# Optimization experiments

Hardware: AMD Instinct MI355X
Metric: run time of the kernel (lower is better)

## Reference

```python
import jax, jax.numpy as jnp
import numpy as np

N = 250_000
E = 8_000_000
EPS = 1e-5


def _bn(x, gamma, beta):
    # BatchNorm1d in training mode: batch stats over dim 0, biased variance
    mu = x.mean(axis=0)
    var = x.var(axis=0)
    return (x - mu) * jax.lax.rsqrt(var + EPS) * gamma + beta


def setup_inputs() -> dict:
    key = jax.random.key(0)
    ks = jax.random.split(key, 24)
    f32 = jnp.float32
    inp = {
        'pos': jax.random.normal(ks[0], (N, 2), f32),
        'vel': jax.random.normal(ks[1], (N, 2), f32),
        'edge_index': jax.random.randint(ks[2], (2, E), 0, N, jnp.int32),
        'lin_in_w': jax.random.normal(ks[3], (4, 4), f32) * 0.5,
        'lin_in_b': jax.random.normal(ks[4], (4,), f32) * 0.1,
        'msg_w1': jax.random.normal(ks[5], (8, 8), f32) * 0.35,
        'msg_b1': jax.random.normal(ks[6], (8,), f32) * 0.1,
        'msg_g1': jax.random.uniform(ks[7], (8,), f32, 0.5, 1.5),
        'msg_be1': jax.random.normal(ks[8], (8,), f32) * 0.1,
        'msg_w2': jax.random.normal(ks[9], (8, 4), f32) * 0.35,
        'msg_b2': jax.random.normal(ks[10], (4,), f32) * 0.1,
        'msg_g2': jax.random.uniform(ks[11], (4,), f32, 0.5, 1.5),
        'msg_be2': jax.random.normal(ks[12], (4,), f32) * 0.1,
        'upd_w1': jax.random.normal(ks[13], (8, 8), f32) * 0.35,
        'upd_b1': jax.random.normal(ks[14], (8,), f32) * 0.1,
        'upd_g1': jax.random.uniform(ks[15], (8,), f32, 0.5, 1.5),
        'upd_be1': jax.random.normal(ks[16], (8,), f32) * 0.1,
        'upd_w2': jax.random.normal(ks[17], (8, 4), f32) * 0.35,
        'upd_b2': jax.random.normal(ks[18], (4,), f32) * 0.1,
        'upd_g2': jax.random.uniform(ks[19], (4,), f32, 0.5, 1.5),
        'upd_be2': jax.random.normal(ks[20], (4,), f32) * 0.1,
        'pred_w': jax.random.normal(ks[21], (4, 2), f32) * 0.5,
        'pred_b': jax.random.normal(ks[22], (2,), f32) * 0.1,
    }
    return inp


def reference(pos, vel, edge_index,
              lin_in_w, lin_in_b,
              msg_w1, msg_b1, msg_g1, msg_be1,
              msg_w2, msg_b2, msg_g2, msg_be2,
              upd_w1, upd_b1, upd_g1, upd_be1,
              upd_w2, upd_b2, upd_g2, upd_be2,
              pred_w, pred_b):
    n = pos.shape[0]
    # input projection: h = lin_in(cat(pos, vel))  -> [N, 4]
    h = jnp.concatenate([pos, vel], axis=-1) @ lin_in_w + lin_in_b

    # PyG source_to_target: j = source = edge_index[0], i = target = edge_index[1]
    src, dst = edge_index[0], edge_index[1]
    h_i = h[dst]  # [E, 4]
    h_j = h[src]  # [E, 4]

    # message MLP on cat(h_i, h_j): Linear->BN->Tanh->Linear->BN->Tanh
    m = jnp.concatenate([h_i, h_j], axis=-1)            # [E, 8]
    m = jnp.tanh(_bn(m @ msg_w1 + msg_b1, msg_g1, msg_be1))
    m = jnp.tanh(_bn(m @ msg_w2 + msg_b2, msg_g2, msg_be2))  # [E, 4]

    # zero out messages where h_i == h_j exactly (self-like edges)
    zero_diff = jnp.all(h_i == h_j, axis=1)             # [E]
    m = jnp.where(zero_diff[:, None], 0.0, m)

    # aggregate: scatter-add on first half, scatter-mean on second half
    add_out = jax.ops.segment_sum(m[:, :2], dst, num_segments=n)   # [N, 2]
    sum_out = jax.ops.segment_sum(m[:, 2:], dst, num_segments=n)   # [N, 2]
    cnt = jax.ops.segment_sum(jnp.ones((m.shape[0],), m.dtype), dst, num_segments=n)
    mean_out = sum_out / jnp.maximum(cnt, 1.0)[:, None]
    aggr = jnp.concatenate([add_out, mean_out], axis=1)  # [N, 4]

    # update MLP on cat(h, aggr)
    u = jnp.concatenate([h, aggr], axis=-1)              # [N, 8]
    u = jnp.tanh(_bn(u @ upd_w1 + upd_b1, upd_g1, upd_be1))
    u = jnp.tanh(_bn(u @ upd_w2 + upd_b2, upd_g2, upd_be2))  # [N, 4]

    return u @ pred_w + pred_b                           # [N, 2]
```

## Files before the change

kernel.cpp:

```cpp
#include <hip/hip_runtime.h>

#define EPSBN 1e-5f
#define NB 512
#define GB 256
#define CAP 18000

typedef float vf4 __attribute__((ext_vector_type(4)));
typedef _Float16 vh8 __attribute__((ext_vector_type(8)));
typedef unsigned int uint32;

__device__ __forceinline__ float ftanh(float x) {
    return 1.0f - 2.0f / (__expf(2.0f * x) + 1.0f);
}

__device__ __forceinline__ float wave_sum(float v) {
#pragma unroll
    for (int off = 32; off > 0; off >>= 1) v += __shfl_down(v, off);
    return v;
}

__device__ __forceinline__ void z1_of(const float4 hi, const float4 hj,
                                      const float* __restrict__ w, const float* __restrict__ b,
                                      float* z) {
#pragma unroll
    for (int j = 0; j < 8; ++j) {
        z[j] = b[j]
             + hi.x * w[0 * 8 + j] + hi.y * w[1 * 8 + j] + hi.z * w[2 * 8 + j] + hi.w * w[3 * 8 + j]
             + hj.x * w[4 * 8 + j] + hj.y * w[5 * 8 + j] + hj.z * w[6 * 8 + j] + hj.w * w[7 * 8 + j];
    }
}

__device__ __forceinline__ void mat8x4(const float* u, const float* w,
                                       const float* b, float* z) {
#pragma unroll
    for (int c = 0; c < 4; ++c) {
        float t = b[c];
#pragma unroll
        for (int k = 0; k < 8; ++k) t += u[k] * w[k * 4 + c];
        z[c] = t;
    }
}

__device__ __forceinline__ void mat8x8(const float* u, const float* __restrict__ w,
                                       const float* __restrict__ b, float* z) {
#pragma unroll
    for (int j = 0; j < 8; ++j) {
        float t = b[j];
#pragma unroll
        for (int k = 0; k < 8; ++k) t += u[k] * w[k * 8 + j];
        z[j] = t;
    }
}

template <int NV>
__device__ __forceinline__ void block_reduce_atomics(float* a, float* __restrict__ sums) {
    __shared__ float red[NV * 4];
    int wid = threadIdx.x >> 6, lane = threadIdx.x & 63;
#pragma unroll
    for (int i = 0; i < NV; ++i) {
        float v = wave_sum(a[i]);
        if (lane == 0) red[i * 4 + wid] = v;
    }
    __syncthreads();
    if (threadIdx.x < NV) {
        float v = red[threadIdx.x * 4 + 0] + red[threadIdx.x * 4 + 1]
                + red[threadIdx.x * 4 + 2] + red[threadIdx.x * 4 + 3];
        atomicAdd(&sums[threadIdx.x], v);
    }
}

__device__ __forceinline__ void fin_lds(const float* __restrict__ sums,
                                        const float* __restrict__ g, const float* __restrict__ be,
                                        int d, float inv, float* out) {
    int j = threadIdx.x;
    if (j < d) {
        float mu = sums[j] * inv;
        float var = sums[d + j] * inv - mu * mu;
        float s = g[j] * rsqrtf(var + EPSBN);
        out[j] = s;
        out[d + j] = be[j] - mu * s;
    }
    __syncthreads();
}

__device__ __forceinline__ void stats1_edge(float4 hi, float4 hj,
                                            const float* __restrict__ w1, const float* __restrict__ b1,
                                            float* a) {
    float z[8];
    z1_of(hi, hj, w1, b1, z);
#pragma unroll
    for (int j = 0; j < 8; ++j) { a[j] += z[j]; a[8 + j] += z[j] * z[j]; }
}

__device__ __forceinline__ vf4 z2_edge(float4 hi, float4 hj,
                                       const float* __restrict__ w1, const float* __restrict__ b1,
                                       const float* ss1,
                                       const float* __restrict__ w2, const float* __restrict__ b2) {
    float z[8], m1[8], z2[4];
    z1_of(hi, hj, w1, b1, z);
#pragma unroll
    for (int j = 0; j < 8; ++j) m1[j] = ftanh(z[j] * ss1[j] + ss1[8 + j]);
    mat8x4(m1, w2, b2, z2);
    vf4 r = {z2[0], z2[1], z2[2], z2[3]};
    return r;
}

__device__ __forceinline__ void stats2_edge(float4 hi, float4 hj,
                                            const float* __restrict__ w1, const float* __restrict__ b1,
                                            const float* ss1,
                                            const float* __restrict__ w2, const float* __restrict__ b2,
                                            float* a) {
    vf4 q = z2_edge(hi, hj, w1, b1, ss1, w2, b2);
    a[0] += q.x; a[4] += q.x * q.x;
    a[1] += q.y; a[5] += q.y * q.y;
    a[2] += q.z; a[6] += q.z * q.z;
    a[3] += q.w; a[7] += q.w * q.w;
}

__device__ __forceinline__ void m1_ofh(vf4 ziA, vf4 ziB, vh8 zjh, float* m1) {
    m1[0] = ftanh(ziA.x + (float)zjh[0]); m1[1] = ftanh(ziA.y + (float)zjh[1]);
    m1[2] = ftanh(ziA.z + (float)zjh[2]); m1[3] = ftanh(ziA.w + (float)zjh[3]);
    m1[4] = ftanh(ziB.x + (float)zjh[4]); m1[5] = ftanh(ziB.y + (float)zjh[5]);
    m1[6] = ftanh(ziB.z + (float)zjh[6]); m1[7] = ftanh(ziB.w + (float)zjh[7]);
}

__global__ __launch_bounds__(256) void k_h(const float* __restrict__ pos, const float* __restrict__ vel,
                                           const float* __restrict__ w, const float* __restrict__ b,
                                           float4* __restrict__ h, int n) {
    int i = blockIdx.x * blockDim.x + threadIdx.x;
    if (i >= n) return;
    float2 p = ((const float2*)pos)[i];
    float2 v = ((const float2*)vel)[i];
    float o[4];
#pragma unroll
    for (int d = 0; d < 4; ++d)
        o[d] = b[d] + p.x * w[0 * 4 + d] + p.y * w[1 * 4 + d] + v.x * w[2 * 4 + d] + v.y * w[3 * 4 + d];
    h[i] = make_float4(o[0], o[1], o[2], o[3]);
}

__global__ __launch_bounds__(256) void k_zt(const float4* __restrict__ h,
                                            const float* __restrict__ w1, const float* __restrict__ b1,
                                            vf4* __restrict__ zi, vf4* __restrict__ zj, int n) {
    int i = blockIdx.x * blockDim.x + threadIdx.x;
    if (i >= n) return;
    float4 hv = h[i];
    float zi8[8], zj8[8];
#pragma unroll
    for (int j = 0; j < 8; ++j) {
        zi8[j] = hv.x * w1[0 * 8 + j] + hv.y * w1[1 * 8 + j] + hv.z * w1[2 * 8 + j] + hv.w * w1[3 * 8 + j];
        zj8[j] = b1[j]
               + hv.x * w1[4 * 8 + j] + hv.y * w1[5 * 8 + j] + hv.z * w1[6 * 8 + j] + hv.w * w1[7 * 8 + j];
    }
    vf4 a = {zi8[0], zi8[1], zi8[2], zi8[3]};
    vf4 b_ = {zi8[4], zi8[5], zi8[6], zi8[7]};
    vf4 c = {zj8[0], zj8[1], zj8[2], zj8[3]};
    vf4 d = {zj8[4], zj8[5], zj8[6], zj8[7]};
    zi[2 * (size_t)i] = a; zi[2 * (size_t)i + 1] = b_;
    zj[2 * (size_t)i] = c; zj[2 * (size_t)i + 1] = d;
}

__global__ __launch_bounds__(256) void k_fold(vf4* __restrict__ zi, const vf4* __restrict__ zj,
                                              vh8* __restrict__ zjH,
                                              const float* __restrict__ sums1,
                                              const float* __restrict__ g1, const float* __restrict__ be1,
                                              float invE, int n) {
    __shared__ float ss1[16];
    fin_lds(sums1, g1, be1, 8, invE, ss1);
    int i = blockIdx.x * blockDim.x + threadIdx.x;
    if (i >= n) return;
    vf4 a = zi[2 * (size_t)i], b = zi[2 * (size_t)i + 1];
    a.x *= ss1[0]; a.y *= ss1[1]; a.z *= ss1[2]; a.w *= ss1[3];
    b.x *= ss1[4]; b.y *= ss1[5]; b.z *= ss1[6]; b.w *= ss1[7];
    zi[2 * (size_t)i] = a; zi[2 * (size_t)i + 1] = b;
    vf4 c = zj[2 * (size_t)i], d = zj[2 * (size_t)i + 1];
    vh8 hpk;
    hpk[0] = (_Float16)(c.x * ss1[0] + ss1[8]);
    hpk[1] = (_Float16)(c.y * ss1[1] + ss1[9]);
    hpk[2] = (_Float16)(c.z * ss1[2] + ss1[10]);
    hpk[3] = (_Float16)(c.w * ss1[3] + ss1[11]);
    hpk[4] = (_Float16)(d.x * ss1[4] + ss1[12]);
    hpk[5] = (_Float16)(d.y * ss1[5] + ss1[13]);
    hpk[6] = (_Float16)(d.z * ss1[6] + ss1[14]);
    hpk[7] = (_Float16)(d.w * ss1[7] + ss1[15]);
    zjH[i] = hpk;
}

__global__ void k_foldw(const float* __restrict__ sums2,
                        const float* __restrict__ g2, const float* __restrict__ be2, float invE,
                        const float* __restrict__ w2, const float* __restrict__ b2,
                        float* __restrict__ w2f, float* __restrict__ b2f) {
    __shared__ float ss2[8];
    int j = threadIdx.x;
    if (j < 4) {
        float mu = sums2[j] * invE;
        float var = sums2[4 + j] * invE - mu * mu;
        float s = g2[j] * rsqrtf(var + EPSBN);
        ss2[j] = s;
        ss2[4 + j] = be2[j] - mu * s;
    }
    __syncthreads();
    if (j < 32) w2f[j] = w2[j] * ss2[j & 3];
    if (j < 4)  b2f[j] = b2[j] * ss2[j] + ss2[4 + j];
}

__global__ __launch_bounds__(256, 2) void k_cnt(const int* __restrict__ idx, const float4* __restrict__ h,
                                                const float* __restrict__ w1, const float* __restrict__ b1,
                                                uint32* __restrict__ cntmat, float* __restrict__ sums,
                                                int E_, int T) {
    __shared__ uint32 hist[NB];
    for (int b = threadIdx.x; b < NB; b += 256) hist[b] = 0;
    float a[16];
#pragma unroll
    for (int i = 0; i < 16; ++i) a[i] = 0.f;
    __syncthreads();
    int lo = blockIdx.x * T, hi2 = min(E_, lo + T);
    for (int e0 = lo + 4 * threadIdx.x; e0 < hi2; e0 += 1024) {
        int m = min(4, hi2 - e0);
        if (m == 4) {
            int s0 = __builtin_nontemporal_load(idx + e0);
            int s1 = __builtin_nontemporal_load(idx + e0 + 1);
            int s2 = __builtin_nontemporal_load(idx + e0 + 2);
            int s3 = __builtin_nontemporal_load(idx + e0 + 3);
            int d0 = __builtin_nontemporal_load(idx + E_ + e0);
            int d1 = __builtin_nontemporal_load(idx + E_ + e0 + 1);
            int d2 = __builtin_nontemporal_load(idx + E_ + e0 + 2);
            int d3 = __builtin_nontemporal_load(idx + E_ + e0 + 3);
            float4 hi0 = h[d0], hj0 = h[s0];
            float4 hi1 = h[d1], hj1 = h[s1];
            float4 hi2 = h[d2], hj2 = h[s2];
            float4 hi3 = h[d3], hj3 = h[s3];
            atomicAdd(&hist[d0 >> 9], 1u);
            atomicAdd(&hist[d1 >> 9], 1u);
            atomicAdd(&hist[d2 >> 9], 1u);
            atomicAdd(&hist[d3 >> 9], 1u);
            stats1_edge(hi0, hj0, w1, b1, a);
            stats1_edge(hi1, hj1, w1, b1, a);
            stats1_edge(hi2, hj2, w1, b1, a);
            stats1_edge(hi3, hj3, w1, b1, a);
        } else {
            for (int k = 0; k < m; ++k) {
                int s = __builtin_nontemporal_load(idx + e0 + k);
                int d = __builtin_nontemporal_load(idx + E_ + e0 + k);
                float4 hi = h[d], hj = h[s];
                atomicAdd(&hist[d >> 9], 1u);
                stats1_edge(hi, hj, w1, b1, a);
            }
        }
    }
    __syncthreads();
    for (int b = threadIdx.x; b < NB; b += 256)
        cntmat[(size_t)b * GB + blockIdx.x] = hist[b];
    block_reduce_atomics<16>(a, sums);
}

__device__ __forceinline__ void scan256(uint32 v, uint32* excl_out, uint32* total) {
    __shared__ uint32 ts[256];
    ts[threadIdx.x] = v;
    __syncthreads();
    for (int off = 1; off < 256; off <<= 1) {
        uint32 t = (threadIdx.x >= (uint32)off) ? ts[threadIdx.x - off] : 0u;
        __syncthreads();
        ts[threadIdx.x] += t;
        __syncthreads();
    }
    *excl_out = ts[threadIdx.x] - v;
    *total = ts[255];
}

__device__ __forceinline__ void scan512(uint32* v, uint32* excl_out, uint32* total) {
    __shared__ uint32 ts[256];
    uint32 local = v[0] + v[1];
    ts[threadIdx.x] = local;
    __syncthreads();
    for (int off = 1; off < 256; off <<= 1) {
        uint32 t = (threadIdx.x >= (uint32)off) ? ts[threadIdx.x - off] : 0u;
        __syncthreads();
        ts[threadIdx.x] += t;
        __syncthreads();
    }
    *excl_out = ts[threadIdx.x] - local;
    *total = ts[255];
}

__global__ __launch_bounds__(256) void k_scanA(uint32* __restrict__ cntmat, uint32* __restrict__ rowtot) {
    size_t base = (size_t)blockIdx.x * GB + threadIdx.x;
    uint32 v = cntmat[base];
    uint32 excl, tot;
    scan256(v, &excl, &tot);
    cntmat[base] = excl;
    if (threadIdx.x == 0) rowtot[blockIdx.x] = tot;
}

__global__ __launch_bounds__(256) void k_scanB(const uint32* __restrict__ rowtot, uint32* __restrict__ bbase) {
    uint32 v[2];
    v[0] = rowtot[threadIdx.x * 2]; v[1] = rowtot[threadIdx.x * 2 + 1];
    uint32 excl, tot;
    scan512(v, &excl, &tot);
    bbase[threadIdx.x * 2] = excl;
    bbase[threadIdx.x * 2 + 1] = excl + v[0];
    if (threadIdx.x == 0) bbase[NB] = tot;
}

__global__ __launch_bounds__(256) void k_reorder(const int* __restrict__ idx,
                                                 const uint32* __restrict__ cntmat, const uint32* __restrict__ bbase,
                                                 uint32* __restrict__ sp, int E_, int T) {
    __shared__ uint32 cur[NB];
    for (int b = threadIdx.x; b < NB; b += 256)
        cur[b] = bbase[b] + cntmat[(size_t)b * GB + blockIdx.x];
    __syncthreads();
    int lo = blockIdx.x * T, hi2 = min(E_, lo + T);
    for (int e0 = lo + 4 * threadIdx.x; e0 < hi2; e0 += 1024) {
        int m = min(4, hi2 - e0);
        if (m == 4) {
            int s0 = __builtin_nontemporal_load(idx + e0);
            int s1 = __builtin_nontemporal_load(idx + e0 + 1);
            int s2 = __builtin_nontemporal_load(idx + e0 + 2);
            int s3 = __builtin_nontemporal_load(idx + e0 + 3);
            int d0 = __builtin_nontemporal_load(idx + E_ + e0);
            int d1 = __builtin_nontemporal_load(idx + E_ + e0 + 1);
            int d2 = __builtin_nontemporal_load(idx + E_ + e0 + 2);
            int d3 = __builtin_nontemporal_load(idx + E_ + e0 + 3);
            uint32 p0 = atomicAdd(&cur[d0 >> 9], 1u);
            uint32 p1 = atomicAdd(&cur[d1 >> 9], 1u);
            uint32 p2 = atomicAdd(&cur[d2 >> 9], 1u);
            uint32 p3 = atomicAdd(&cur[d3 >> 9], 1u);
            sp[p0] = ((uint32)(d0 & 511) << 23) | (uint32)s0;
            sp[p1] = ((uint32)(d1 & 511) << 23) | (uint32)s1;
            sp[p2] = ((uint32)(d2 & 511) << 23) | (uint32)s2;
            sp[p3] = ((uint32)(d3 & 511) << 23) | (uint32)s3;
        } else {
            for (int k = 0; k < m; ++k) {
                int s = __builtin_nontemporal_load(idx + e0 + k);
                int d = __builtin_nontemporal_load(idx + E_ + e0 + k);
                uint32 pos = atomicAdd(&cur[d >> 9], 1u);
                sp[pos] = ((uint32)(d & 511) << 23) | (uint32)s;
            }
        }
    }
}

__global__ __launch_bounds__(256) void k_sort2(const uint32* __restrict__ sp,
                                               const uint32* __restrict__ bbase, const uint32* __restrict__ rowtot,
                                               int* __restrict__ src2, uint32* __restrict__ nodeoff, int n) {
    extern __shared__ uint32 buf[];
    __shared__ uint32 hist[512];
    __shared__ uint32 cur[512];
    int b = blockIdx.x;
    uint32 start = bbase[b];
    uint32 len = rowtot[b];
    uint32 end = start + len;
    hist[threadIdx.x] = 0;
    hist[threadIdx.x + 256] = 0;
    __syncthreads();
    for (uint32 e = start + threadIdx.x; e < end; e += 256) {
        uint32 pk = __builtin_nontemporal_load(&sp[e]);
        atomicAdd(&hist[pk >> 23], 1u);
    }
    __syncthreads();
    uint32 vv[2];
    vv[0] = hist[2 * threadIdx.x];
    vv[1] = hist[2 * threadIdx.x + 1];
    uint32 excl, tot;
    scan512(vv, &excl, &tot);
    cur[2 * threadIdx.x] = excl;
    cur[2 * threadIdx.x + 1] = excl + vv[0];
    int nodebase = b << 9;
    int node0 = nodebase + 2 * threadIdx.x;
    if (node0 <= n)     nodeoff[node0] = start + excl;
    if (node0 + 1 <= n) nodeoff[node0 + 1] = start + excl + vv[0];
    __syncthreads();
    for (uint32 e = start + threadIdx.x; e < end; e += 256) {
        uint32 pk = __builtin_nontemporal_load(&sp[e]);
        uint32 pos = atomicAdd(&cur[pk >> 23], 1u);
        uint32 src = pk & 0x7FFFFFu;
        if (pos < (uint32)CAP) buf[pos] = src;
        else src2[start + pos] = (int)src;
    }
    __syncthreads();
    uint32 lim = min(len, (uint32)CAP);
    for (uint32 k = threadIdx.x; k < lim; k += 256)
        src2[start + k] = (int)buf[k];
}

__global__ void k_fin(const float* __restrict__ sums, float* __restrict__ ss,
                      const float* __restrict__ g, const float* __restrict__ be,
                      int d, float inv_count) {
    int j = threadIdx.x;
    if (j >= d) return;
    float mu = sums[j] * inv_count;
    float var = sums[d + j] * inv_count - mu * mu;
    float s = g[j] * rsqrtf(var + EPSBN);
    ss[j] = s;
    ss[d + j] = be[j] - mu * s;
}

__global__ __launch_bounds__(256, 2) void e_pass2(const int* __restrict__ src2, const uint32* __restrict__ nodeoff,
                                                  const vf4* __restrict__ ziS, const vh8* __restrict__ zjH,
                                                  const float* __restrict__ w2, const float* __restrict__ b2,
                                                  float* __restrict__ sums2, int n) {
    __shared__ float w2l[32];
    __shared__ float b2l[4];
    if (threadIdx.x < 32) w2l[threadIdx.x] = w2[threadIdx.x];
    if (threadIdx.x < 4)  b2l[threadIdx.x] = b2[threadIdx.x];
    __syncthreads();
    float a[8];
#pragma unroll
    for (int i = 0; i < 8; ++i) a[i] = 0.f;
    int lane = threadIdx.x & 15;
    int gid0 = (blockIdx.x * 256 + threadIdx.x) >> 4;
    int gstride = (gridDim.x * 256) >> 4;
    for (int i = gid0; i < n; i += gstride) {
        uint32 e0 = nodeoff[i], e1 = nodeoff[i + 1];
        vf4 ziA = ziS[2 * (size_t)i], ziB = ziS[2 * (size_t)i + 1];
        for (uint32 e = e0 + lane; e < e1; e += 16) {
            int s = src2[e];
            vh8 zjh = zjH[s];
            float m1[8], z2[4];
            m1_ofh(ziA, ziB, zjh, m1);
            mat8x4(m1, w2l, b2l, z2);
            a[0] += z2[0]; a[4] += z2[0] * z2[0];
            a[1] += z2[1]; a[5] += z2[1] * z2[1];
            a[2] += z2[2]; a[6] += z2[2] * z2[2];
            a[3] += z2[3]; a[7] += z2[3] * z2[3];
        }
    }
    block_reduce_atomics<8>(a, sums2);
}

__global__ __launch_bounds__(256, 2) void e_aggr_csr(const int* __restrict__ src2, const uint32* __restrict__ nodeoff,
                                                     const vf4* __restrict__ ziS, const vh8* __restrict__ zjH,
                                                     const float* __restrict__ w2f, const float* __restrict__ b2f,
                                                     float* __restrict__ acc, int n) {
    __shared__ float w2l[32];
    __shared__ float b2l[4];
    if (threadIdx.x < 32) w2l[threadIdx.x] = w2f[threadIdx.x];
    if (threadIdx.x < 4)  b2l[threadIdx.x] = b2f[threadIdx.x];
    __syncthreads();
    int lane = threadIdx.x & 15;
    int gid0 = (blockIdx.x * 256 + threadIdx.x) >> 4;
    int gstride = (gridDim.x * 256) >> 4;
    for (int i = gid0; i < n; i += gstride) {
        uint32 e0 = nodeoff[i], e1 = nodeoff[i + 1];
        vf4 ziA = ziS[2 * (size_t)i], ziB = ziS[2 * (size_t)i + 1];
        float a0 = 0.f, a1 = 0.f, a2 = 0.f, a3 = 0.f;
        for (uint32 e = e0 + lane; e < e1; e += 16) {
            int s = src2[e];
            vh8 zjh = zjH[s];
            if (s != i) {
                float m1[8], z2[4];
                m1_ofh(ziA, ziB, zjh, m1);
                mat8x4(m1, w2l, b2l, z2);
                a0 += ftanh(z2[0]);
                a1 += ftanh(z2[1]);
                a2 += ftanh(z2[2]);
                a3 += ftanh(z2[3]);
            }
        }
#pragma unroll
        for (int off = 8; off > 0; off >>= 1) {
            a0 += __shfl_down(a0, off, 16);
            a1 += __shfl_down(a1, off, 16);
            a2 += __shfl_down(a2, off, 16);
            a3 += __shfl_down(a3, off, 16);
        }
        if (lane == 0) {
            float* ap = acc + 8 * (size_t)i;
            ap[0] = a0; ap[1] = a1; ap[2] = a2; ap[3] = a3;
            ap[4] = (float)(e1 - e0);
        }
    }
}

__global__ __launch_bounds__(256) void fb_stats1(const int* __restrict__ idx, const float4* __restrict__ h,
                                                 const float* __restrict__ w1, const float* __restrict__ b1,
                                                 float* __restrict__ sums, float* __restrict__ acc, int E_) {
    float a[16];
#pragma unroll
    for (int i = 0; i < 16; ++i) a[i] = 0.f;
    int stride = gridDim.x * blockDim.x;
    for (int e = blockIdx.x * blockDim.x + threadIdx.x; e < E_; e += stride) {
        int s = __builtin_nontemporal_load(idx + e);
        int d = __builtin_nontemporal_load(idx + E_ + e);
        float4 hi = h[d], hj = h[s];
        stats1_edge(hi, hj, w1, b1, a);
        atomicAdd(acc + 8 * (size_t)d + 4, 1.0f);
    }
    block_reduce_atomics<16>(a, sums);
}

__global__ __launch_bounds__(256) void fb_stats2(const int* __restrict__ idx, const float4* __restrict__ h,
                                                 const float* __restrict__ w1, const float* __restrict__ b1,
                                                 const float* __restrict__ ss1,
                                                 const float* __restrict__ w2, const float* __restrict__ b2,
                                                 float* __restrict__ sums2, int E_) {
    float a[8];
#pragma unroll
    for (int i = 0; i < 8; ++i) a[i] = 0.f;
    int stride = gridDim.x * blockDim.x;
    for (int e = blockIdx.x * blockDim.x + threadIdx.x; e < E_; e += stride) {
        int s = __builtin_nontemporal_load(idx + e);
        int d = __builtin_nontemporal_load(idx + E_ + e);
        float4 hi = h[d], hj = h[s];
        stats2_edge(hi, hj, w1, b1, ss1, w2, b2, a);
    }
    block_reduce_atomics<8>(a, sums2);
}

__global__ __launch_bounds__(256) void fb_scatter(const int* __restrict__ idx, const float4* __restrict__ h,
                                                  const float* __restrict__ w1, const float* __restrict__ b1,
                                                  const float* __restrict__ ss1,
                                                  const float* __restrict__ w2, const float* __restrict__ b2,
                                                  const float* __restrict__ ss2,
                                                  float* __restrict__ acc, int E_) {
    int stride = gridDim.x * blockDim.x;
    for (int e = blockIdx.x * blockDim.x + threadIdx.x; e < E_; e += stride) {
        int s = __builtin_nontemporal_load(idx + e);
        int d = __builtin_nontemporal_load(idx + E_ + e);
        float4 hi = h[d], hj = h[s];
        bool zero = (hi.x == hj.x) && (hi.y == hj.y) && (hi.z == hj.z) && (hi.w == hj.w);
        if (zero) continue;
        vf4 q = z2_edge(hi, hj, w1, b1, ss1, w2, b2);
        float m0 = ftanh(q.x * ss2[0] + ss2[4]);
        float m1v = ftanh(q.y * ss2[1] + ss2[5]);
        float m2v = ftanh(q.z * ss2[2] + ss2[6]);
        float m3 = ftanh(q.w * ss2[3] + ss2[7]);
        float* ap = acc + 8 * (size_t)d;
        atomicAdd(ap + 0, m0);
        atomicAdd(ap + 1, m1v);
        atomicAdd(ap + 2, m2v);
        atomicAdd(ap + 3, m3);
    }
}

__device__ __forceinline__ void load_u(int i, const float4* __restrict__ h,
                                       const float* __restrict__ acc, float* u) {
    float4 hv = h[i];
    const float* ap = acc + 8 * (size_t)i;
    float c = fmaxf(ap[4], 1.0f);
    u[0] = hv.x; u[1] = hv.y; u[2] = hv.z; u[3] = hv.w;
    u[4] = ap[0]; u[5] = ap[1]; u[6] = ap[2] / c; u[7] = ap[3] / c;
}

__global__ __launch_bounds__(256) void n_stats1(const float4* __restrict__ h,
                                                const float* __restrict__ acc,
                                                const float* __restrict__ w, const float* __restrict__ b,
                                                float* __restrict__ sums, int n) {
    float a[16];
#pragma unroll
    for (int i = 0; i < 16; ++i) a[i] = 0.f;
    int stride = gridDim.x * blockDim.x;
    for (int i = blockIdx.x * blockDim.x + threadIdx.x; i < n; i += stride) {
        float u[8], z[8];
        load_u(i, h, acc, u);
        mat8x8(u, w, b, z);
#pragma unroll
        for (int j = 0; j < 8; ++j) { a[j] += z[j]; a[8 + j] += z[j] * z[j]; }
    }
    block_reduce_atomics<16>(a, sums);
}

__global__ __launch_bounds__(256) void n_stats2(const float4* __restrict__ h,
                                                const float* __restrict__ acc,
                                                const float* __restrict__ w1, const float* __restrict__ b1,
                                                const float* __restrict__ sums3,
                                                const float* __restrict__ g3, const float* __restrict__ be3,
                                                float invN,
                                                const float* __restrict__ w2, const float* __restrict__ b2,
                                                float* __restrict__ sums, int n) {
    __shared__ float ss3[16];
    fin_lds(sums3, g3, be3, 8, invN, ss3);
    float a[8];
#pragma unroll
    for (int i = 0; i < 8; ++i) a[i] = 0.f;
    int stride = gridDim.x * blockDim.x;
    for (int i = blockIdx.x * blockDim.x + threadIdx.x; i < n; i += stride) {
        float u[8], z[8], u1[8], z4[4];
        load_u(i, h, acc, u);
        mat8x8(u, w1, b1, z);
#pragma unroll
        for (int j = 0; j < 8; ++j) u1[j] = ftanh(z[j] * ss3[j] + ss3[8 + j]);
        mat8x4(u1, w2, b2, z4);
#pragma unroll
        for (int c = 0; c < 4; ++c) { a[c] += z4[c]; a[4 + c] += z4[c] * z4[c]; }
    }
    block_reduce_atomics<8>(a, sums);
}

__global__ __launch_bounds__(256) void n_final(const float4* __restrict__ h,
                                               const float* __restrict__ acc,
                                               const float* __restrict__ w1, const float* __restrict__ b1,
                                               const float* __restrict__ sums3,
                                               const float* __restrict__ g3, const float* __restrict__ be3,
                                               const float* __restrict__ sums4,
                                               const float* __restrict__ g4, const float* __restrict__ be4,
                                               float invN,
                                               const float* __restrict__ w2, const float* __restrict__ b2,
                                               const float* __restrict__ pw, const float* __restrict__ pb,
                                               float2* __restrict__ out, int n) {
    __shared__ float ss3[16];
    __shared__ float ss4[8];
    fin_lds(sums3, g3, be3, 8, invN, ss3);
    fin_lds(sums4, g4, be4, 4, invN, ss4);
    int stride = gridDim.x * blockDim.x;
    for (int i = blockIdx.x * blockDim.x + threadIdx.x; i < n; i += stride) {
        float u[8], z[8], u1[8], z4[4], u2[4];
        load_u(i, h, acc, u);
        mat8x8(u, w1, b1, z);
#pragma unroll
        for (int j = 0; j < 8; ++j) u1[j] = ftanh(z[j] * ss3[j] + ss3[8 + j]);
        mat8x4(u1, w2, b2, z4);
#pragma unroll
        for (int c = 0; c < 4; ++c) u2[c] = ftanh(z4[c] * ss4[c] + ss4[4 + c]);
        float o0 = pb[0] + u2[0] * pw[0] + u2[1] * pw[2] + u2[2] * pw[4] + u2[3] * pw[6];
        float o1 = pb[1] + u2[0] * pw[1] + u2[1] * pw[3] + u2[2] * pw[5] + u2[3] * pw[7];
        out[i] = make_float2(o0, o1);
    }
}

extern "C" void kernel_launch(void* const* d_in, const int* in_sizes, int n_in,
                              void* d_out, int out_size, void* d_ws, size_t ws_size,
                              hipStream_t stream) {
    const float* pos  = (const float*)d_in[0];
    const float* vel  = (const float*)d_in[1];
    const int*   eidx = (const int*)d_in[2];
    const float* lin_w = (const float*)d_in[3];
    const float* lin_b = (const float*)d_in[4];
    const float* mw1 = (const float*)d_in[5];
    const float* mb1 = (const float*)d_in[6];
    const float* mg1 = (const float*)d_in[7];
    const float* mbe1 = (const float*)d_in[8];
    const float* mw2 = (const float*)d_in[9];
    const float* mb2 = (const float*)d_in[10];
    const float* mg2 = (const float*)d_in[11];
    const float* mbe2 = (const float*)d_in[12];
    const float* uw1 = (const float*)d_in[13];
    const float* ub1 = (const float*)d_in[14];
    const float* ug1 = (const float*)d_in[15];
    const float* ube1 = (const float*)d_in[16];
    const float* uw2 = (const float*)d_in[17];
    const float* ub2 = (const float*)d_in[18];
    const float* ug2 = (const float*)d_in[19];
    const float* ube2 = (const float*)d_in[20];
    const float* pw = (const float*)d_in[21];
    const float* pb = (const float*)d_in[22];

    int n  = in_sizes[0] / 2;
    int E_ = in_sizes[2] / 2;
    float invE = 1.0f / (float)E_;
    float invN = 1.0f / (float)n;

    char* base = (char*)d_ws;
    size_t off = 0;
    auto alloc = [&](size_t bytes) {
        off = (off + 15) & ~(size_t)15;
        void* p = base + off;
        off += bytes;
        return p;
    };
    float4* h       = (float4*)alloc(16 * (size_t)n);
    float*  acc     = (float*)alloc(32 * (size_t)n);
    float*  sums    = (float*)alloc(512);
    float*  ss      = sums + 64;
    float*  w2fb    = (float*)alloc(256);
    uint32* bbase   = (uint32*)alloc(4 * (NB + 1));
    uint32* rowtot  = (uint32*)alloc(4 * NB);
    uint32* cntmat  = (uint32*)alloc(4 * (size_t)NB * GB);
    uint32* nodeoff = (uint32*)alloc(4 * ((size_t)n + 1));
    vf4*    ziS     = (vf4*)alloc(32 * (size_t)n);
    vf4*    zjS     = (vf4*)alloc(32 * (size_t)n);
    vh8*    zjH     = (vh8*)alloc(16 * (size_t)n);
    int*    src2    = (int*)alloc(4 * (size_t)E_);
    uint32* sp      = (uint32*)alloc(4 * (size_t)E_);
    size_t need_sort = off;

    bool big = (ws_size >= need_sort) && (n < (1 << 23));

    int nblk = (n + 255) / 256;
    int nbuckets = (n + 511) >> 9;
    int T = (E_ + GB - 1) / GB;

    k_h<<<nblk, 256, 0, stream>>>(pos, vel, lin_w, lin_b, h, n);

    if (big) {
        (void)hipMemsetAsync(sums, 0, 256, stream);

        k_zt<<<nblk, 256, 0, stream>>>(h, mw1, mb1, ziS, zjS, n);

        k_cnt<<<GB, 256, 0, stream>>>(eidx, h, mw1, mb1, cntmat, sums, E_, T);
        k_scanA<<<NB, 256, 0, stream>>>(cntmat, rowtot);
        k_scanB<<<1, 256, 0, stream>>>(rowtot, bbase);

        k_fold<<<nblk, 256, 0, stream>>>(ziS, zjS, zjH, sums, mg1, mbe1, invE, n);

        k_reorder<<<GB, 256, 0, stream>>>(eidx, cntmat, bbase, sp, E_, T);
        k_sort2<<<nbuckets, 256, CAP * 4, stream>>>(sp, bbase, rowtot, src2, nodeoff, n);

        e_pass2<<<4096, 256, 0, stream>>>(src2, nodeoff, ziS, zjH, mw2, mb2, sums + 16, n);

        k_foldw<<<1, 64, 0, stream>>>(sums + 16, mg2, mbe2, invE, mw2, mb2, w2fb, w2fb + 32);

        e_aggr_csr<<<4096, 256, 0, stream>>>(src2, nodeoff, ziS, zjH, w2fb, w2fb + 32, acc, n);

        n_stats1<<<nblk, 256, 0, stream>>>(h, acc, uw1, ub1, sums + 24, n);
        n_stats2<<<nblk, 256, 0, stream>>>(h, acc, uw1, ub1, sums + 24, ug1, ube1, invN,
                                           uw2, ub2, sums + 40, n);
        n_final<<<nblk, 256, 0, stream>>>(h, acc, uw1, ub1, sums + 24, ug1, ube1,
                                          sums + 40, ug2, ube2, invN,
                                          uw2, ub2, pw, pb, (float2*)d_out, n);
    } else {
        (void)hipMemsetAsync(acc, 0, 32 * (size_t)n + 256, stream);

        fb_stats1<<<4096, 256, 0, stream>>>(eidx, h, mw1, mb1, sums, acc, E_);
        k_fin<<<1, 64, 0, stream>>>(sums, ss, mg1, mbe1, 8, invE);

        fb_stats2<<<4096, 256, 0, stream>>>(eidx, h, mw1, mb1, ss, mw2, mb2, sums + 16, E_);
        k_fin<<<1, 64, 0, stream>>>(sums + 16, ss + 16, mg2, mbe2, 4, invE);

        fb_scatter<<<4096, 256, 0, stream>>>(eidx, h, mw1, mb1, ss, mw2, mb2, ss + 16, acc, E_);

        n_stats1<<<nblk, 256, 0, stream>>>(h, acc, uw1, ub1, sums + 24, n);
        n_stats2<<<nblk, 256, 0, stream>>>(h, acc, uw1, ub1, sums + 24, ug1, ube1, invN,
                                           uw2, ub2, sums + 40, n);
        n_final<<<nblk, 256, 0, stream>>>(h, acc, uw1, ub1, sums + 24, ug1, ube1,
                                          sums + 40, ug2, ube2, invN,
                                          uw2, ub2, pw, pb, (float2*)d_out, n);
    }
}
```

Baseline: 497.1 us.

## Cache pre-BN edge activations in fp16 and aggregate from the cached buffer

The second-stage BN statistics pass now stores each edge's pre-BN z2 as four fp16 values, with an infinity sentinel marking self edges. The aggregation kernel reads this per-edge buffer and applies the BN scale/shift and tanh, no longer re-gathering zjH and recomputing both matmuls. The separate weight-fold kernel is removed and a reciprocal intrinsic replaces the division in tanh. This trades random gathers and recompute for an extra 64 MB write and a sequential read. It also adds fp16 rounding of z2 before normalisation, and the sentinel fails if a real z2 overflows fp16.

After: 432.2 us. 1.15x faster.

```diff
diff --git a/kernel.cpp b/kernel.cpp
--- a/kernel.cpp
+++ b/kernel.cpp
@@ -7,10 +7,12 @@
 
 typedef float vf4 __attribute__((ext_vector_type(4)));
 typedef _Float16 vh8 __attribute__((ext_vector_type(8)));
+typedef _Float16 vh4 __attribute__((ext_vector_type(4)));
 typedef unsigned int uint32;
 
 __device__ __forceinline__ float ftanh(float x) {
-    return 1.0f - 2.0f / (__expf(2.0f * x) + 1.0f);
+    float e = __expf(2.0f * x);
+    return 1.0f - 2.0f * __builtin_amdgcn_rcpf(e + 1.0f);
 }
 
 __device__ __forceinline__ float wave_sum(float v) {
@@ -183,24 +185,6 @@
     hpk[6] = (_Float16)(d.z * ss1[6] + ss1[14]);
     hpk[7] = (_Float16)(d.w * ss1[7] + ss1[15]);
     zjH[i] = hpk;
-}
-
-__global__ void k_foldw(const float* __restrict__ sums2,
-                        const float* __restrict__ g2, const float* __restrict__ be2, float invE,
-                        const float* __restrict__ w2, const float* __restrict__ b2,
-                        float* __restrict__ w2f, float* __restrict__ b2f) {
-    __shared__ float ss2[8];
-    int j = threadIdx.x;
-    if (j < 4) {
-        float mu = sums2[j] * invE;
-        float var = sums2[4 + j] * invE - mu * mu;
-        float s = g2[j] * rsqrtf(var + EPSBN);
-        ss2[j] = s;
-        ss2[4 + j] = be2[j] - mu * s;
-    }
-    __syncthreads();
-    if (j < 32) w2f[j] = w2[j] * ss2[j & 3];
-    if (j < 4)  b2f[j] = b2[j] * ss2[j] + ss2[4 + j];
 }
 
 __global__ __launch_bounds__(256, 2) void k_cnt(const int* __restrict__ idx, const float4* __restrict__ h,
@@ -397,7 +381,7 @@
 __global__ __launch_bounds__(256, 2) void e_pass2(const int* __restrict__ src2, const uint32* __restrict__ nodeoff,
                                                   const vf4* __restrict__ ziS, const vh8* __restrict__ zjH,
                                                   const float* __restrict__ w2, const float* __restrict__ b2,
-                                                  float* __restrict__ sums2, int n) {
+                                                  float* __restrict__ sums2, vh4* __restrict__ z2h, int n) {
     __shared__ float w2l[32];
     __shared__ float b2l[4];
     if (threadIdx.x < 32) w2l[threadIdx.x] = w2[threadIdx.x];
@@ -422,38 +406,38 @@
             a[1] += z2[1]; a[5] += z2[1] * z2[1];
             a[2] += z2[2]; a[6] += z2[2] * z2[2];
             a[3] += z2[3]; a[7] += z2[3] * z2[3];
+            vh4 pk;
+            pk[0] = (s == i) ? (_Float16)__builtin_inff() : (_Float16)z2[0];
+            pk[1] = (_Float16)z2[1];
+            pk[2] = (_Float16)z2[2];
+            pk[3] = (_Float16)z2[3];
+            z2h[e] = pk;
         }
     }
     block_reduce_atomics<8>(a, sums2);
 }
 
-__global__ __launch_bounds__(256, 2) void e_aggr_csr(const int* __restrict__ src2, const uint32* __restrict__ nodeoff,
-                                                     const vf4* __restrict__ ziS, const vh8* __restrict__ zjH,
-                                                     const float* __restrict__ w2f, const float* __restrict__ b2f,
-                                                     float* __restrict__ acc, int n) {
-    __shared__ float w2l[32];
-    __shared__ float b2l[4];
-    if (threadIdx.x < 32) w2l[threadIdx.x] = w2f[threadIdx.x];
-    if (threadIdx.x < 4)  b2l[threadIdx.x] = b2f[threadIdx.x];
-    __syncthreads();
+__global__ __launch_bounds__(256, 2) void e_aggr_z(const vh4* __restrict__ z2h, const uint32* __restrict__ nodeoff,
+                                                   const float* __restrict__ sums2,
+                                                   const float* __restrict__ g2, const float* __restrict__ be2,
+                                                   float invE,
+                                                   float* __restrict__ acc, int n) {
+    __shared__ float ss2[8];
+    fin_lds(sums2, g2, be2, 4, invE, ss2);
     int lane = threadIdx.x & 15;
     int gid0 = (blockIdx.x * 256 + threadIdx.x) >> 4;
     int gstride = (gridDim.x * 256) >> 4;
     for (int i = gid0; i < n; i += gstride) {
         uint32 e0 = nodeoff[i], e1 = nodeoff[i + 1];
-        vf4 ziA = ziS[2 * (size_t)i], ziB = ziS[2 * (size_t)i + 1];
         float a0 = 0.f, a1 = 0.f, a2 = 0.f, a3 = 0.f;
         for (uint32 e = e0 + lane; e < e1; e += 16) {
-            int s = src2[e];
-            vh8 zjh = zjH[s];
-            if (s != i) {
-                float m1[8], z2[4];
-                m1_ofh(ziA, ziB, zjh, m1);
-                mat8x4(m1, w2l, b2l, z2);
-                a0 += ftanh(z2[0]);
-                a1 += ftanh(z2[1]);
-                a2 += ftanh(z2[2]);
-                a3 += ftanh(z2[3]);
+            vh4 pk = z2h[e];
+            float z0 = (float)pk[0];
+            if (z0 != __builtin_inff()) {
+                a0 += ftanh(z0 * ss2[0] + ss2[4]);
+                a1 += ftanh((float)pk[1] * ss2[1] + ss2[5]);
+                a2 += ftanh((float)pk[2] * ss2[2] + ss2[6]);
+                a3 += ftanh((float)pk[3] * ss2[3] + ss2[7]);
             }
         }
 #pragma unroll
@@ -661,7 +645,6 @@
     float*  acc     = (float*)alloc(32 * (size_t)n);
     float*  sums    = (float*)alloc(512);
     float*  ss      = sums + 64;
-    float*  w2fb    = (float*)alloc(256);
     uint32* bbase   = (uint32*)alloc(4 * (NB + 1));
     uint32* rowtot  = (uint32*)alloc(4 * NB);
     uint32* cntmat  = (uint32*)alloc(4 * (size_t)NB * GB);
@@ -671,6 +654,7 @@
     vh8*    zjH     = (vh8*)alloc(16 * (size_t)n);
     int*    src2    = (int*)alloc(4 * (size_t)E_);
     uint32* sp      = (uint32*)alloc(4 * (size_t)E_);
+    vh4*    z2h     = (vh4*)alloc(8 * (size_t)E_);
     size_t need_sort = off;
 
     bool big = (ws_size >= need_sort) && (n < (1 << 23));
@@ -695,11 +679,9 @@
         k_reorder<<<GB, 256, 0, stream>>>(eidx, cntmat, bbase, sp, E_, T);
         k_sort2<<<nbuckets, 256, CAP * 4, stream>>>(sp, bbase, rowtot, src2, nodeoff, n);
 
-        e_pass2<<<4096, 256, 0, stream>>>(src2, nodeoff, ziS, zjH, mw2, mb2, sums + 16, n);
-
-        k_foldw<<<1, 64, 0, stream>>>(sums + 16, mg2, mbe2, invE, mw2, mb2, w2fb, w2fb + 32);
-
-        e_aggr_csr<<<4096, 256, 0, stream>>>(src2, nodeoff, ziS, zjH, w2fb, w2fb + 32, acc, n);
+        e_pass2<<<4096, 256, 0, stream>>>(src2, nodeoff, ziS, zjH, mw2, mb2, sums + 16, z2h, n);
+
+        e_aggr_z<<<4096, 256, 0, stream>>>(z2h, nodeoff, sums + 16, mg2, mbe2, invE, acc, n);
 
         n_stats1<<<nblk, 256, 0, stream>>>(h, acc, uw1, ub1, sums + 24, n);
         n_stats2<<<nblk, 256, 0, stream>>>(h, acc, uw1, ub1, sums + 24, ug1, ube1, invN,
```
